# Performance work log

Hardware: AMD Instinct MI355X
Metric: run time of the kernel (lower is better)

Reference implementation:

```python
import jax, jax.numpy as jnp
import numpy as np

D_MODEL = 256
NUM_HEADS = 8
WINDOW = 7
B, H, W = 2, 56, 56


def setup_inputs() -> dict:
    key = jax.random.key(0)
    ks = jax.random.split(key, 9)
    s = D_MODEL ** -0.5
    return {
        "x": jax.random.normal(ks[0], (B, D_MODEL, H, W), jnp.float32),
        "wq": jax.random.normal(ks[1], (D_MODEL, D_MODEL), jnp.float32) * s,
        "bq": jnp.zeros((D_MODEL,), jnp.float32),
        "wk": jax.random.normal(ks[2], (D_MODEL, D_MODEL), jnp.float32) * s,
        "bk": jnp.zeros((D_MODEL,), jnp.float32),
        "wv": jax.random.normal(ks[3], (D_MODEL, D_MODEL), jnp.float32) * s,
        "bv": jnp.zeros((D_MODEL,), jnp.float32),
        "wo": jax.random.normal(ks[4], (D_MODEL, D_MODEL), jnp.float32) * s,
        "bo": jnp.zeros((D_MODEL,), jnp.float32),
    }


def _proj(x, w, b):
    # 1x1 conv == channel matmul. x: [B,C,H,W], w: [Cout,Cin], b: [Cout]
    return jnp.einsum('oc,bchw->bohw', w, x) + b[None, :, None, None]


def _windows(t, ws):
    # t: [B,h,d,H,W] -> [B,h,d,H,W,ws*ws], zero-padded sliding windows.
    # Row-major (i*ws + j) flattening matches torch unfold(3).unfold(4).view(...,-1).
    pad = ws // 2
    Hh, Ww = t.shape[-2], t.shape[-1]
    tp = jnp.pad(t, ((0, 0), (0, 0), (0, 0), (pad, pad), (pad, pad)))
    return jnp.stack([tp[..., i:i + Hh, j:j + Ww]
                      for i in range(ws) for j in range(ws)], axis=-1)


def reference(x, wq, bq, wk, bk, wv, bv, wo, bo):
    Bt, C, Hh, Ww = x.shape
    hd = C // NUM_HEADS
    scale = hd ** -0.5
    q = _proj(x, wq, bq).reshape(Bt, NUM_HEADS, hd, Hh, Ww)
    k = _proj(x, wk, bk).reshape(Bt, NUM_HEADS, hd, Hh, Ww)
    v = _proj(x, wv, bv).reshape(Bt, NUM_HEADS, hd, Hh, Ww)
    kw = _windows(k, WINDOW)  # [B,h,d,H,W,ws^2]
    vw = _windows(v, WINDOW)
    attn = jnp.einsum('bhdxy,bhdxyw->bhxyw', q, kw) * scale
    attn = jax.nn.softmax(attn, axis=-1)
    out = jnp.einsum('bhxyw,bhdxyw->bhdxy', attn, vw).reshape(Bt, C, Hh, Ww)
    return _proj(out, wo, bo)
```

## Files before the change

kernel.cpp:

```cpp
#include <hip/hip_runtime.h>
#include <hip/hip_bf16.h>
#include <cstdint>

#define NHEAD 8
#define HD 32
#define DM 256
#define HH 56
#define WWID 56
#define HW 3136
#define NB 2
#define NTOT (NB * HW)
#define SCALE 0.17677669529663687f

typedef _Float16 f16;
typedef __attribute__((ext_vector_type(2))) _Float16 f16x2;
typedef __attribute__((ext_vector_type(8))) _Float16 f16x8;
typedef __attribute__((ext_vector_type(4))) float floatx4;

union U16 { uint4 u; f16x2 h2[4]; f16 h[8]; };

__global__ __launch_bounds__(256) void prep(
    const float* __restrict__ x,
    const float* __restrict__ wq, const float* __restrict__ wk,
    const float* __restrict__ wv, const float* __restrict__ wo,
    f16* __restrict__ xT, f16* __restrict__ wcat, f16* __restrict__ wob)
{
    const int bid = blockIdx.x;
    const int t = threadIdx.x;
    if (bid < 392) {
        __shared__ float tile[64][65];
        const int b = bid / 196, r = bid - b * 196;
        const int ct = r / 49, pt = r - ct * 49;
        const int p0 = pt * 64, c0 = ct * 64;
        const float* xb = x + (size_t)b * DM * HW;
        #pragma unroll
        for (int i = 0; i < 4; ++i) {
            const int u = t + i * 256;
            const int rc = u >> 4, p4 = (u & 15) << 2;
            *(float4*)&tile[rc][p4] =
                *(const float4*)&xb[(size_t)(c0 + rc) * HW + p0 + p4];
        }
        __syncthreads();
        f16* xo = xT + (size_t)b * HW * DM;
        #pragma unroll
        for (int i = 0; i < 2; ++i) {
            const int u = t + i * 256;
            const int ch = u & 7, p = u >> 3;
            U16 pk;
            #pragma unroll
            for (int kk = 0; kk < 8; ++kk)
                pk.h[kk] = (f16)tile[ch * 8 + kk][p];
            *(uint4*)&xo[(size_t)(p0 + p) * DM + c0 + ch * 8] = pk.u;
        }
    } else {
        const int gid = (bid - 392) * 256 + t;
        const int idx4 = gid << 2;
        const int sel = idx4 >> 16;
        const int off = idx4 & 65535;
        const float* src = sel == 0 ? wq : (sel == 1 ? wk : (sel == 2 ? wv : wo));
        f16* dst = sel < 3 ? (wcat + (sel << 16) + off) : (wob + off);
        float4 f = *(const float4*)&src[off];
        union { ushort4 u; f16 h[4]; } pk;
        pk.h[0] = (f16)f.x; pk.h[1] = (f16)f.y;
        pk.h[2] = (f16)f.z; pk.h[3] = (f16)f.w;
        *(ushort4*)dst = pk.u;
    }
}

template<int MODE>
__global__ __launch_bounds__(256) void gemm_mfma(
    const f16* __restrict__ A,
    const f16* __restrict__ Bm,
    const float* __restrict__ b0, const float* __restrict__ b1,
    const float* __restrict__ b2,
    void* __restrict__ o0, void* __restrict__ o1, void* __restrict__ o2)
{
    const int n0 = blockIdx.x * 64;
    const int m0 = blockIdx.y * 128;
    const int bb = n0 / HW;
    const int np = n0 - bb * HW;
    const f16* Bb = Bm + (size_t)n0 * DM;

    __shared__ __align__(16) f16 As[128][72];
    __shared__ __align__(16) f16 Bs[64][72];

    const int t = threadIdx.x;
    const int wave = t >> 6, lane = t & 63;
    const int quad = lane >> 4, l16 = lane & 15;
    const int mw = (wave & 1) * 64, nw = (wave >> 1) * 32;

    floatx4 acc[4][2] = {};

    const int srow = t >> 3, suc = (t & 7) << 3;

    for (int k0 = 0; k0 < DM; k0 += 64) {
        #pragma unroll
        for (int pp = 0; pp < 4; ++pp) {
            const int row = srow + pp * 32;
            *(uint4*)&As[row][suc] =
                *(const uint4*)&A[(size_t)(m0 + row) * DM + k0 + suc];
        }
        #pragma unroll
        for (int pp = 0; pp < 2; ++pp) {
            const int row = srow + pp * 32;
            *(uint4*)&Bs[row][suc] =
                *(const uint4*)&Bb[(size_t)row * DM + k0 + suc];
        }
        __syncthreads();
        #pragma unroll
        for (int ks = 0; ks < 2; ++ks) {
            f16x8 af[4], bf[2];
            #pragma unroll
            for (int mt = 0; mt < 4; ++mt)
                af[mt] = *(const f16x8*)&As[mw + mt * 16 + l16][ks * 32 + quad * 8];
            #pragma unroll
            for (int nt = 0; nt < 2; ++nt)
                bf[nt] = *(const f16x8*)&Bs[nw + nt * 16 + l16][ks * 32 + quad * 8];
            #pragma unroll
            for (int mt = 0; mt < 4; ++mt)
                #pragma unroll
                for (int nt = 0; nt < 2; ++nt)
                    acc[mt][nt] = __builtin_amdgcn_mfma_f32_16x16x32_f16(
                        af[mt], bf[nt], acc[mt][nt], 0, 0, 0);
        }
        __syncthreads();
    }

    if (MODE == 0) {
        #pragma unroll
        for (int mt = 0; mt < 4; ++mt) {
            const int gm = m0 + mw + mt * 16 + quad * 4;
            const int proj = gm >> 8;
            const int c = gm & 255;
            const int h = c >> 5, d0 = c & 31;
            const float* bptr = proj == 0 ? b0 : (proj == 1 ? b1 : b2);
            f16* op = (f16*)(proj == 0 ? o0 : (proj == 1 ? o1 : o2));
            const float sc = proj == 0 ? SCALE : 1.0f;
            const size_t base = ((size_t)(bb * NHEAD + h) * HW) * HD + d0;
            float bias[4] = {bptr[c], bptr[c + 1], bptr[c + 2], bptr[c + 3]};
            #pragma unroll
            for (int nt = 0; nt < 2; ++nt) {
                const int p = np + nw + nt * 16 + l16;
                union { ushort4 u; f16 h[4]; } pk;
                #pragma unroll
                for (int r = 0; r < 4; ++r)
                    pk.h[r] = (f16)((acc[mt][nt][r] + bias[r]) * sc);
                *(ushort4*)&op[base + (size_t)p * HD] = pk.u;
            }
        }
    } else {
        float* yo = (float*)o0;
        #pragma unroll
        for (int mt = 0; mt < 4; ++mt) {
            const int gc = m0 + mw + mt * 16 + quad * 4;
            #pragma unroll
            for (int r = 0; r < 4; ++r) {
                const float bias = b0[gc + r];
                #pragma unroll
                for (int nt = 0; nt < 2; ++nt) {
                    const int p = np + nw + nt * 16 + l16;
                    yo[(size_t)(bb * DM + gc + r) * HW + p] = acc[mt][nt][r] + bias;
                }
            }
        }
    }
}

#define HROWS 8
#define HPOS  (HROWS * WWID)
#define HPP   (HPOS + 6)

__global__ __launch_bounds__(448) void attn_win(
    const f16* __restrict__ q,
    const f16* __restrict__ k,
    const f16* __restrict__ v,
    f16* __restrict__ out)
{
    __shared__ uint4 kh[HPP * 4];
    __shared__ uint4 vh[HPP * 4];

    const int t = threadIdx.x;
    const int tile = blockIdx.x;
    const int h = blockIdx.y, b = blockIdx.z;
    const int y0 = tile * 2;
    const size_t base = (size_t)(b * NHEAD + h) * HW * HD;
    const f16* kp = k + base;
    const f16* vp = v + base;

    #pragma unroll
    for (int it = 0; it < 4; ++it) {
        const int u = t + it * 448;
        const int pos = u >> 2, ch = u & 3;
        const int hr = pos / WWID;
        const int gx = pos - hr * WWID;
        const int gy = y0 - 3 + hr;
        uint4 kv = make_uint4(0, 0, 0, 0), vv = make_uint4(0, 0, 0, 0);
        if ((unsigned)gy < HH) {
            const size_t g = (size_t)(gy * WWID + gx) * HD + (ch << 3);
            kv = *(const uint4*)&kp[g];
            vv = *(const uint4*)&vp[g];
        }
        kh[u + 12] = kv;
        vh[u + 12] = vv;
    }
    if (t < 48) {
        const int ps = t % 6;
        const int fi = (ps < 3 ? ps * 4 : (HPOS + ps) * 4) + ((t / 6) & 3);
        const uint4 z = make_uint4(0, 0, 0, 0);
        if (t < 24) kh[fi] = z; else vh[fi] = z;
    }
    __syncthreads();

    const int pl = t >> 2;
    const int ch = t & 3;
    const int lx = pl >= WWID ? pl - WWID : pl;
    const int p = y0 * WWID + pl;

    U16 qu;
    qu.u = *(const uint4*)(q + base + (size_t)p * HD + (ch << 3));

    const uint4* kb4 = kh + t;
    const uint4* vb4 = vh + t;

    float of[8] = {};
    float sum = 0.f;
    for (int i = 0; i < 7; ++i) {
        #pragma unroll
        for (int j = 0; j < 7; ++j) {
            const int off4 = (i * WWID + j) << 2;
            U16 ku; ku.u = kb4[off4];
            float s;
            s = __builtin_amdgcn_fdot2(ku.h2[0], qu.h2[0], 0.0f, false);
            s = __builtin_amdgcn_fdot2(ku.h2[1], qu.h2[1], s, false);
            s = __builtin_amdgcn_fdot2(ku.h2[2], qu.h2[2], s, false);
            s = __builtin_amdgcn_fdot2(ku.h2[3], qu.h2[3], s, false);
            s += __shfl_xor(s, 1);
            s += __shfl_xor(s, 2);
            const bool xv = (unsigned)(lx + j - 3) < WWID;
            const float e = __expf(s);
            sum += xv ? e : 1.0f;
            const float wt = xv ? e : 0.0f;
            U16 vu; vu.u = vb4[off4];
            of[0] = fmaf((float)vu.h[0], wt, of[0]);
            of[1] = fmaf((float)vu.h[1], wt, of[1]);
            of[2] = fmaf((float)vu.h[2], wt, of[2]);
            of[3] = fmaf((float)vu.h[3], wt, of[3]);
            of[4] = fmaf((float)vu.h[4], wt, of[4]);
            of[5] = fmaf((float)vu.h[5], wt, of[5]);
            of[6] = fmaf((float)vu.h[6], wt, of[6]);
            of[7] = fmaf((float)vu.h[7], wt, of[7]);
        }
    }

    const float inv = 1.0f / sum;
    f16* op = out + ((size_t)b * HW + p) * DM + h * HD + (ch << 3);
    U16 ou;
    #pragma unroll
    for (int j = 0; j < 8; ++j)
        ou.h[j] = (f16)(of[j] * inv);
    *(uint4*)op = ou.u;
}

extern "C" void kernel_launch(void* const* d_in, const int* in_sizes, int n_in,
                              void* d_out, int out_size, void* d_ws, size_t ws_size,
                              hipStream_t stream) {
    const float* x  = (const float*)d_in[0];
    const float* wq = (const float*)d_in[1];
    const float* bq = (const float*)d_in[2];
    const float* wk = (const float*)d_in[3];
    const float* bk = (const float*)d_in[4];
    const float* wv = (const float*)d_in[5];
    const float* bv = (const float*)d_in[6];
    const float* wo = (const float*)d_in[7];
    const float* bo = (const float*)d_in[8];
    float* out = (float*)d_out;

    const size_t NPC = (size_t)NTOT * DM;
    f16* xT    = (f16*)d_ws;
    f16* wcat  = xT + NPC;
    f16* wob   = wcat + 768 * 256;
    f16* qb    = wob + 256 * 256;
    f16* kb    = qb + NPC;
    f16* vb    = kb + NPC;
    f16* attnT = vb + NPC;

    prep<<<648, 256, 0, stream>>>(x, wq, wk, wv, wo, xT, wcat, wob);
    gemm_mfma<0><<<dim3(NTOT / 64, 6), 256, 0, stream>>>(
        wcat, xT, bq, bk, bv, qb, kb, vb);
    attn_win<<<dim3(28, NHEAD, NB), 448, 0, stream>>>(qb, kb, vb, attnT);
    gemm_mfma<1><<<dim3(NTOT / 64, 2), 256, 0, stream>>>(
        wob, attnT, bo, bo, bo, out, out, out);
}
```

Before: 113.4 us.

## Fuse all four stages into one persistent kernel with software grid barriers

Replaces the four launches (prep, QKV GEMM, windowed attention, output GEMM) with a single persistent 512-block kernel that separates the phases with a hierarchical atomic grid barrier. The attention phase also moves from 2-row strips to 8x8 spatial tiles with a 14x14 zero-padded halo, which removes the per-column validity masking. The aim is to cut kernel launch gaps and tail effects between stages. In exchange, the GEMMs now loop over tiles within a fixed grid, the barrier spins add cost, and correctness relies on all 512 blocks being co-resident, since block 0 resets the barrier state while other blocks may already be spinning on it.

```diff
diff --git a/kernel.cpp b/kernel.cpp
--- a/kernel.cpp
+++ b/kernel.cpp
@@ -11,6 +11,9 @@
 #define NB 2
 #define NTOT (NB * HW)
 #define SCALE 0.17677669529663687f
+#define NBLK 512
+#define GEN0 0x13570000u
+#define AGT __HIP_MEMORY_SCOPE_AGENT
 
 typedef _Float16 f16;
 typedef __attribute__((ext_vector_type(2))) _Float16 f16x2;
@@ -19,16 +22,148 @@
 
 union U16 { uint4 u; f16x2 h2[4]; f16 h[8]; };
 
-__global__ __launch_bounds__(256) void prep(
+__device__ __forceinline__ void gridsync(unsigned* bar, unsigned expect) {
+    __syncthreads();
+    if (threadIdx.x == 0) {
+        unsigned* gen = bar + 288;
+        while (__hip_atomic_load(gen, __ATOMIC_ACQUIRE, AGT) != expect) {}
+        __threadfence();
+        unsigned* cg = bar + ((blockIdx.x >> 6) << 5);
+        if (__hip_atomic_fetch_add(cg, 1u, __ATOMIC_ACQ_REL, AGT) == 63u) {
+            __hip_atomic_store(cg, 0u, __ATOMIC_RELAXED, AGT);
+            unsigned* root = bar + 256;
+            if (__hip_atomic_fetch_add(root, 1u, __ATOMIC_ACQ_REL, AGT) == 7u) {
+                __hip_atomic_store(root, 0u, __ATOMIC_RELAXED, AGT);
+                __hip_atomic_store(gen, expect + 1u, __ATOMIC_RELEASE, AGT);
+            } else {
+                while (__hip_atomic_load(gen, __ATOMIC_ACQUIRE, AGT) == expect) {}
+            }
+        } else {
+            while (__hip_atomic_load(gen, __ATOMIC_ACQUIRE, AGT) == expect) {}
+        }
+        __threadfence();
+    }
+    __syncthreads();
+}
+
+template<int MODE>
+__device__ __forceinline__ void gemm_phase(
+    const f16* __restrict__ A, const f16* __restrict__ Bm,
+    const float* __restrict__ b0, const float* __restrict__ b1,
+    const float* __restrict__ b2,
+    f16* __restrict__ o0, f16* __restrict__ o1, f16* __restrict__ o2,
+    float* __restrict__ yo,
+    void* smem, int ntiles)
+{
+    f16 (*As)[72] = (f16(*)[72])smem;
+    f16 (*Bs)[72] = (f16(*)[72])((char*)smem + 18432);
+    const int t = threadIdx.x;
+    const int wave = t >> 6, lane = t & 63;
+    const int quad = lane >> 4, l16 = lane & 15;
+    const int mw = (wave & 1) * 64, nw = (wave >> 1) * 32;
+    const int srow = t >> 3, suc = (t & 7) << 3;
+
+    for (int tile = blockIdx.x; tile < ntiles; tile += NBLK) {
+        const int mt = tile / 98, nt = tile - mt * 98;
+        const int n0g = nt * 64, m0 = mt * 128;
+        const int bb = n0g / HW, np = n0g - bb * HW;
+        const f16* Bb = Bm + (size_t)n0g * DM;
+        floatx4 acc[4][2] = {};
+        for (int k0 = 0; k0 < DM; k0 += 64) {
+            #pragma unroll
+            for (int pp = 0; pp < 4; ++pp) {
+                const int row = srow + pp * 32;
+                *(uint4*)&As[row][suc] =
+                    *(const uint4*)&A[(size_t)(m0 + row) * DM + k0 + suc];
+            }
+            #pragma unroll
+            for (int pp = 0; pp < 2; ++pp) {
+                const int row = srow + pp * 32;
+                *(uint4*)&Bs[row][suc] =
+                    *(const uint4*)&Bb[(size_t)row * DM + k0 + suc];
+            }
+            __syncthreads();
+            #pragma unroll
+            for (int ks = 0; ks < 2; ++ks) {
+                f16x8 af[4], bf[2];
+                #pragma unroll
+                for (int mt2 = 0; mt2 < 4; ++mt2)
+                    af[mt2] = *(const f16x8*)&As[mw + mt2 * 16 + l16][ks * 32 + quad * 8];
+                #pragma unroll
+                for (int nt2 = 0; nt2 < 2; ++nt2)
+                    bf[nt2] = *(const f16x8*)&Bs[nw + nt2 * 16 + l16][ks * 32 + quad * 8];
+                #pragma unroll
+                for (int mt2 = 0; mt2 < 4; ++mt2)
+                    #pragma unroll
+                    for (int nt2 = 0; nt2 < 2; ++nt2)
+                        acc[mt2][nt2] = __builtin_amdgcn_mfma_f32_16x16x32_f16(
+                            af[mt2], bf[nt2], acc[mt2][nt2], 0, 0, 0);
+            }
+            __syncthreads();
+        }
+        if (MODE == 0) {
+            #pragma unroll
+            for (int mt2 = 0; mt2 < 4; ++mt2) {
+                const int gm = m0 + mw + mt2 * 16 + quad * 4;
+                const int proj = gm >> 8;
+                const int c = gm & 255;
+                const int h = c >> 5, d0 = c & 31;
+                const float* bptr = proj == 0 ? b0 : (proj == 1 ? b1 : b2);
+                f16* op = proj == 0 ? o0 : (proj == 1 ? o1 : o2);
+                const float sc = proj == 0 ? SCALE : 1.0f;
+                const size_t base = ((size_t)(bb * NHEAD + h) * HW) * HD + d0;
+                float bias[4] = {bptr[c], bptr[c + 1], bptr[c + 2], bptr[c + 3]};
+                #pragma unroll
+                for (int nt2 = 0; nt2 < 2; ++nt2) {
+                    const int p = np + nw + nt2 * 16 + l16;
+                    union { ushort4 u; f16 h[4]; } pk;
+                    #pragma unroll
+                    for (int r = 0; r < 4; ++r)
+                        pk.h[r] = (f16)((acc[mt2][nt2][r] + bias[r]) * sc);
+                    *(ushort4*)&op[base + (size_t)p * HD] = pk.u;
+                }
+            }
+        } else {
+            #pragma unroll
+            for (int mt2 = 0; mt2 < 4; ++mt2) {
+                const int gc = m0 + mw + mt2 * 16 + quad * 4;
+                #pragma unroll
+                for (int r = 0; r < 4; ++r) {
+                    const float bias = b0[gc + r];
+                    #pragma unroll
+                    for (int nt2 = 0; nt2 < 2; ++nt2) {
+                        const int p = np + nw + nt2 * 16 + l16;
+                        yo[(size_t)(bb * DM + gc + r) * HW + p] = acc[mt2][nt2][r] + bias;
+                    }
+                }
+            }
+        }
+    }
+}
+
+__global__ __launch_bounds__(256) void fused_all(
     const float* __restrict__ x,
-    const float* __restrict__ wq, const float* __restrict__ wk,
-    const float* __restrict__ wv, const float* __restrict__ wo,
-    f16* __restrict__ xT, f16* __restrict__ wcat, f16* __restrict__ wob)
+    const float* __restrict__ wq, const float* __restrict__ bq,
+    const float* __restrict__ wk, const float* __restrict__ bk,
+    const float* __restrict__ wv, const float* __restrict__ bv,
+    const float* __restrict__ wo, const float* __restrict__ bo,
+    f16* __restrict__ xT, f16* __restrict__ wcat, f16* __restrict__ wob,
+    f16* __restrict__ qb, f16* __restrict__ kb, f16* __restrict__ vb,
+    f16* __restrict__ attnT, float* __restrict__ out, unsigned* bar)
 {
-    const int bid = blockIdx.x;
-    const int t = threadIdx.x;
+    __shared__ __align__(16) unsigned char smem[27648];
+    const int bid = blockIdx.x, t = threadIdx.x;
+
+    if (bid == 0 && t == 0) {
+        #pragma unroll
+        for (int g = 0; g < 8; ++g)
+            __hip_atomic_store(bar + g * 32, 0u, __ATOMIC_RELAXED, AGT);
+        __hip_atomic_store(bar + 256, 0u, __ATOMIC_RELAXED, AGT);
+        __hip_atomic_store(bar + 288, GEN0, __ATOMIC_RELEASE, AGT);
+    }
+
     if (bid < 392) {
-        __shared__ float tile[64][65];
+        float (*tile)[65] = (float(*)[65])smem;
         const int b = bid / 196, r = bid - b * 196;
         const int ct = r / 49, pt = r - ct * 49;
         const int p0 = pt * 64, c0 = ct * 64;
@@ -45,220 +180,101 @@
         #pragma unroll
         for (int i = 0; i < 2; ++i) {
             const int u = t + i * 256;
-            const int ch = u & 7, p = u >> 3;
+            const int ch = u & 7, pq = u >> 3;
             U16 pk;
             #pragma unroll
             for (int kk = 0; kk < 8; ++kk)
-                pk.h[kk] = (f16)tile[ch * 8 + kk][p];
-            *(uint4*)&xo[(size_t)(p0 + p) * DM + c0 + ch * 8] = pk.u;
+                pk.h[kk] = (f16)tile[ch * 8 + kk][pq];
+            *(uint4*)&xo[(size_t)(p0 + pq) * DM + c0 + ch * 8] = pk.u;
         }
     } else {
-        const int gid = (bid - 392) * 256 + t;
-        const int idx4 = gid << 2;
-        const int sel = idx4 >> 16;
-        const int off = idx4 & 65535;
-        const float* src = sel == 0 ? wq : (sel == 1 ? wk : (sel == 2 ? wv : wo));
-        f16* dst = sel < 3 ? (wcat + (sel << 16) + off) : (wob + off);
-        float4 f = *(const float4*)&src[off];
-        union { ushort4 u; f16 h[4]; } pk;
-        pk.h[0] = (f16)f.x; pk.h[1] = (f16)f.y;
-        pk.h[2] = (f16)f.z; pk.h[3] = (f16)f.w;
-        *(ushort4*)dst = pk.u;
-    }
-}
-
-template<int MODE>
-__global__ __launch_bounds__(256) void gemm_mfma(
-    const f16* __restrict__ A,
-    const f16* __restrict__ Bm,
-    const float* __restrict__ b0, const float* __restrict__ b1,
-    const float* __restrict__ b2,
-    void* __restrict__ o0, void* __restrict__ o1, void* __restrict__ o2)
-{
-    const int n0 = blockIdx.x * 64;
-    const int m0 = blockIdx.y * 128;
-    const int bb = n0 / HW;
-    const int np = n0 - bb * HW;
-    const f16* Bb = Bm + (size_t)n0 * DM;
-
-    __shared__ __align__(16) f16 As[128][72];
-    __shared__ __align__(16) f16 Bs[64][72];
-
-    const int t = threadIdx.x;
-    const int wave = t >> 6, lane = t & 63;
-    const int quad = lane >> 4, l16 = lane & 15;
-    const int mw = (wave & 1) * 64, nw = (wave >> 1) * 32;
-
-    floatx4 acc[4][2] = {};
-
-    const int srow = t >> 3, suc = (t & 7) << 3;
-
-    for (int k0 = 0; k0 < DM; k0 += 64) {
-        #pragma unroll
-        for (int pp = 0; pp < 4; ++pp) {
-            const int row = srow + pp * 32;
-            *(uint4*)&As[row][suc] =
-                *(const uint4*)&A[(size_t)(m0 + row) * DM + k0 + suc];
-        }
-        #pragma unroll
-        for (int pp = 0; pp < 2; ++pp) {
-            const int row = srow + pp * 32;
-            *(uint4*)&Bs[row][suc] =
-                *(const uint4*)&Bb[(size_t)row * DM + k0 + suc];
-        }
-        __syncthreads();
-        #pragma unroll
-        for (int ks = 0; ks < 2; ++ks) {
-            f16x8 af[4], bf[2];
-            #pragma unroll
-            for (int mt = 0; mt < 4; ++mt)
-                af[mt] = *(const f16x8*)&As[mw + mt * 16 + l16][ks * 32 + quad * 8];
-            #pragma unroll
-            for (int nt = 0; nt < 2; ++nt)
-                bf[nt] = *(const f16x8*)&Bs[nw + nt * 16 + l16][ks * 32 + quad * 8];
-            #pragma unroll
-            for (int mt = 0; mt < 4; ++mt)
-                #pragma unroll
-                for (int nt = 0; nt < 2; ++nt)
-                    acc[mt][nt] = __builtin_amdgcn_mfma_f32_16x16x32_f16(
-                        af[mt], bf[nt], acc[mt][nt], 0, 0, 0);
-        }
-        __syncthreads();
-    }
-
-    if (MODE == 0) {
-        #pragma unroll
-        for (int mt = 0; mt < 4; ++mt) {
-            const int gm = m0 + mw + mt * 16 + quad * 4;
-            const int proj = gm >> 8;
-            const int c = gm & 255;
-            const int h = c >> 5, d0 = c & 31;
-            const float* bptr = proj == 0 ? b0 : (proj == 1 ? b1 : b2);
-            f16* op = (f16*)(proj == 0 ? o0 : (proj == 1 ? o1 : o2));
-            const float sc = proj == 0 ? SCALE : 1.0f;
-            const size_t base = ((size_t)(bb * NHEAD + h) * HW) * HD + d0;
-            float bias[4] = {bptr[c], bptr[c + 1], bptr[c + 2], bptr[c + 3]};
-            #pragma unroll
-            for (int nt = 0; nt < 2; ++nt) {
-                const int p = np + nw + nt * 16 + l16;
-                union { ushort4 u; f16 h[4]; } pk;
-                #pragma unroll
-                for (int r = 0; r < 4; ++r)
-                    pk.h[r] = (f16)((acc[mt][nt][r] + bias[r]) * sc);
-                *(ushort4*)&op[base + (size_t)p * HD] = pk.u;
-            }
-        }
-    } else {
-        float* yo = (float*)o0;
-        #pragma unroll
-        for (int mt = 0; mt < 4; ++mt) {
-            const int gc = m0 + mw + mt * 16 + quad * 4;
-            #pragma unroll
-            for (int r = 0; r < 4; ++r) {
-                const float bias = b0[gc + r];
-                #pragma unroll
-                for (int nt = 0; nt < 2; ++nt) {
-                    const int p = np + nw + nt * 16 + l16;
-                    yo[(size_t)(bb * DM + gc + r) * HW + p] = acc[mt][nt][r] + bias;
+        for (int gid = (bid - 392) * 256 + t; gid < 65536; gid += 30720) {
+            const int idx4 = gid << 2;
+            const int sel = idx4 >> 16, off = idx4 & 65535;
+            const float* src = sel == 0 ? wq : (sel == 1 ? wk : (sel == 2 ? wv : wo));
+            f16* dst = sel < 3 ? (wcat + (sel << 16) + off) : (wob + off);
+            float4 f = *(const float4*)&src[off];
+            union { ushort4 u; f16 h[4]; } pk;
+            pk.h[0] = (f16)f.x; pk.h[1] = (f16)f.y;
+            pk.h[2] = (f16)f.z; pk.h[3] = (f16)f.w;
+            *(ushort4*)dst = pk.u;
+        }
+    }
+    gridsync(bar, GEN0);
+
+    gemm_phase<0>(wcat, xT, bq, bk, bv, qb, kb, vb, nullptr, smem, 588);
+    gridsync(bar, GEN0 + 1);
+
+    {
+        uint4* kh = (uint4*)smem;
+        uint4* vh = (uint4*)(smem + 12544);
+        for (int tl = bid; tl < 784; tl += NBLK) {
+            const int bh = tl / 49, r = tl - bh * 49;
+            const int ry = r / 7;
+            const int ty0 = ry * 8, tx0 = (r - ry * 7) * 8;
+            const f16* kp = kb + (size_t)bh * HW * HD;
+            const f16* vp = vb + (size_t)bh * HW * HD;
+            __syncthreads();
+            for (int u = t; u < 784; u += 256) {
+                const int pos = u >> 2, ch = u & 3;
+                const int hy = pos / 14, hx = pos - hy * 14;
+                const int gy = ty0 + hy - 3, gx = tx0 + hx - 3;
+                uint4 kv = make_uint4(0, 0, 0, 0), vv = make_uint4(0, 0, 0, 0);
+                if ((unsigned)gy < HH && (unsigned)gx < WWID) {
+                    const size_t g = (size_t)(gy * WWID + gx) * HD + (ch << 3);
+                    kv = *(const uint4*)&kp[g];
+                    vv = *(const uint4*)&vp[g];
                 }
-            }
-        }
-    }
-}
-
-#define HROWS 8
-#define HPOS  (HROWS * WWID)
-#define HPP   (HPOS + 6)
-
-__global__ __launch_bounds__(448) void attn_win(
-    const f16* __restrict__ q,
-    const f16* __restrict__ k,
-    const f16* __restrict__ v,
-    f16* __restrict__ out)
-{
-    __shared__ uint4 kh[HPP * 4];
-    __shared__ uint4 vh[HPP * 4];
-
-    const int t = threadIdx.x;
-    const int tile = blockIdx.x;
-    const int h = blockIdx.y, b = blockIdx.z;
-    const int y0 = tile * 2;
-    const size_t base = (size_t)(b * NHEAD + h) * HW * HD;
-    const f16* kp = k + base;
-    const f16* vp = v + base;
-
-    #pragma unroll
-    for (int it = 0; it < 4; ++it) {
-        const int u = t + it * 448;
-        const int pos = u >> 2, ch = u & 3;
-        const int hr = pos / WWID;
-        const int gx = pos - hr * WWID;
-        const int gy = y0 - 3 + hr;
-        uint4 kv = make_uint4(0, 0, 0, 0), vv = make_uint4(0, 0, 0, 0);
-        if ((unsigned)gy < HH) {
-            const size_t g = (size_t)(gy * WWID + gx) * HD + (ch << 3);
-            kv = *(const uint4*)&kp[g];
-            vv = *(const uint4*)&vp[g];
-        }
-        kh[u + 12] = kv;
-        vh[u + 12] = vv;
-    }
-    if (t < 48) {
-        const int ps = t % 6;
-        const int fi = (ps < 3 ? ps * 4 : (HPOS + ps) * 4) + ((t / 6) & 3);
-        const uint4 z = make_uint4(0, 0, 0, 0);
-        if (t < 24) kh[fi] = z; else vh[fi] = z;
-    }
-    __syncthreads();
-
-    const int pl = t >> 2;
-    const int ch = t & 3;
-    const int lx = pl >= WWID ? pl - WWID : pl;
-    const int p = y0 * WWID + pl;
-
-    U16 qu;
-    qu.u = *(const uint4*)(q + base + (size_t)p * HD + (ch << 3));
-
-    const uint4* kb4 = kh + t;
-    const uint4* vb4 = vh + t;
-
-    float of[8] = {};
-    float sum = 0.f;
-    for (int i = 0; i < 7; ++i) {
-        #pragma unroll
-        for (int j = 0; j < 7; ++j) {
-            const int off4 = (i * WWID + j) << 2;
-            U16 ku; ku.u = kb4[off4];
-            float s;
-            s = __builtin_amdgcn_fdot2(ku.h2[0], qu.h2[0], 0.0f, false);
-            s = __builtin_amdgcn_fdot2(ku.h2[1], qu.h2[1], s, false);
-            s = __builtin_amdgcn_fdot2(ku.h2[2], qu.h2[2], s, false);
-            s = __builtin_amdgcn_fdot2(ku.h2[3], qu.h2[3], s, false);
-            s += __shfl_xor(s, 1);
-            s += __shfl_xor(s, 2);
-            const bool xv = (unsigned)(lx + j - 3) < WWID;
-            const float e = __expf(s);
-            sum += xv ? e : 1.0f;
-            const float wt = xv ? e : 0.0f;
-            U16 vu; vu.u = vb4[off4];
-            of[0] = fmaf((float)vu.h[0], wt, of[0]);
-            of[1] = fmaf((float)vu.h[1], wt, of[1]);
-            of[2] = fmaf((float)vu.h[2], wt, of[2]);
-            of[3] = fmaf((float)vu.h[3], wt, of[3]);
-            of[4] = fmaf((float)vu.h[4], wt, of[4]);
-            of[5] = fmaf((float)vu.h[5], wt, of[5]);
-            of[6] = fmaf((float)vu.h[6], wt, of[6]);
-            of[7] = fmaf((float)vu.h[7], wt, of[7]);
-        }
-    }
-
-    const float inv = 1.0f / sum;
-    f16* op = out + ((size_t)b * HW + p) * DM + h * HD + (ch << 3);
-    U16 ou;
-    #pragma unroll
-    for (int j = 0; j < 8; ++j)
-        ou.h[j] = (f16)(of[j] * inv);
-    *(uint4*)op = ou.u;
+                kh[u] = kv; vh[u] = vv;
+            }
+            __syncthreads();
+            const int pl = t >> 2, ch = t & 3;
+            const int ty = pl >> 3, tx = pl & 7;
+            const int p = (ty0 + ty) * WWID + tx0 + tx;
+            U16 qu;
+            qu.u = *(const uint4*)(qb + (size_t)bh * HW * HD + (size_t)p * HD + (ch << 3));
+            const uint4* kbase = kh + (ty * 14 + tx) * 4 + ch;
+            const uint4* vbase = vh + (ty * 14 + tx) * 4 + ch;
+            float of[8] = {};
+            float sum = 0.f;
+            for (int i = 0; i < 7; ++i) {
+                #pragma unroll
+                for (int j = 0; j < 7; ++j) {
+                    const int off = (i * 14 + j) << 2;
+                    U16 ku; ku.u = kbase[off];
+                    float s = __builtin_amdgcn_fdot2(ku.h2[0], qu.h2[0], 0.0f, false);
+                    s = __builtin_amdgcn_fdot2(ku.h2[1], qu.h2[1], s, false);
+                    s = __builtin_amdgcn_fdot2(ku.h2[2], qu.h2[2], s, false);
+                    s = __builtin_amdgcn_fdot2(ku.h2[3], qu.h2[3], s, false);
+                    s += __shfl_xor(s, 1);
+                    s += __shfl_xor(s, 2);
+                    const float e = __expf(s);
+                    sum += e;
+                    U16 vu; vu.u = vbase[off];
+                    of[0] = fmaf((float)vu.h[0], e, of[0]);
+                    of[1] = fmaf((float)vu.h[1], e, of[1]);
+                    of[2] = fmaf((float)vu.h[2], e, of[2]);
+                    of[3] = fmaf((float)vu.h[3], e, of[3]);
+                    of[4] = fmaf((float)vu.h[4], e, of[4]);
+                    of[5] = fmaf((float)vu.h[5], e, of[5]);
+                    of[6] = fmaf((float)vu.h[6], e, of[6]);
+                    of[7] = fmaf((float)vu.h[7], e, of[7]);
+                }
+            }
+            const float inv = 1.0f / sum;
+            f16* op = attnT + ((size_t)(bh >> 3) * HW + p) * DM
+                            + (bh & 7) * HD + (ch << 3);
+            U16 ou;
+            #pragma unroll
+            for (int j = 0; j < 8; ++j)
+                ou.h[j] = (f16)(of[j] * inv);
+            *(uint4*)op = ou.u;
+        }
+    }
+    gridsync(bar, GEN0 + 2);
+
+    gemm_phase<1>(wob, attnT, bo, nullptr, nullptr,
+                  nullptr, nullptr, nullptr, out, smem, 196);
 }
 
 extern "C" void kernel_launch(void* const* d_in, const int* in_sizes, int n_in,
@@ -283,11 +299,9 @@
     f16* kb    = qb + NPC;
     f16* vb    = kb + NPC;
     f16* attnT = vb + NPC;
-
-    prep<<<648, 256, 0, stream>>>(x, wq, wk, wv, wo, xT, wcat, wob);
-    gemm_mfma<0><<<dim3(NTOT / 64, 6), 256, 0, stream>>>(
-        wcat, xT, bq, bk, bv, qb, kb, vb);
-    attn_win<<<dim3(28, NHEAD, NB), 448, 0, stream>>>(qb, kb, vb, attnT);
-    gemm_mfma<1><<<dim3(NTOT / 64, 2), 256, 0, stream>>>(
-        wob, attnT, bo, bo, bo, out, out, out);
+    unsigned* bar = (unsigned*)(attnT + NPC);
+
+    fused_all<<<NBLK, 256, 0, stream>>>(
+        x, wq, bq, wk, bk, wv, bv, wo, bo,
+        xT, wcat, wob, qb, kb, vb, attnT, out, bar);
 }
```

After: 303.9 us. +168.1%, slower.

## Fuse fp32-to-fp16 conversion and transpose into the projection GEMMs, dropping prep kernel

Applied to the files above, without the earlier changes.

Removes the separate prep kernel that converted x and the weights to fp16 and transposed x. The QKV GEMM now reads fp32 weights and the NCHW x directly, converting to fp16 while staging into shared memory with a transposed scalar store. The output GEMM likewise converts wo on the fly. This saves one launch and the workspace round trip, but adds redundant weight conversion per block, scalar strided loads of x, and possible bank conflicts on the transposed shared-memory writes.

```diff
diff --git a/kernel.cpp b/kernel.cpp
--- a/kernel.cpp
+++ b/kernel.cpp
@@ -19,67 +19,23 @@
 
 union U16 { uint4 u; f16x2 h2[4]; f16 h[8]; };
 
-__global__ __launch_bounds__(256) void prep(
+__global__ __launch_bounds__(256) void gemm_qkv(
     const float* __restrict__ x,
-    const float* __restrict__ wq, const float* __restrict__ wk,
-    const float* __restrict__ wv, const float* __restrict__ wo,
-    f16* __restrict__ xT, f16* __restrict__ wcat, f16* __restrict__ wob)
+    const float* __restrict__ wq, const float* __restrict__ bq,
+    const float* __restrict__ wk, const float* __restrict__ bk,
+    const float* __restrict__ wv, const float* __restrict__ bv,
+    f16* __restrict__ qo, f16* __restrict__ ko, f16* __restrict__ vo)
 {
-    const int bid = blockIdx.x;
-    const int t = threadIdx.x;
-    if (bid < 392) {
-        __shared__ float tile[64][65];
-        const int b = bid / 196, r = bid - b * 196;
-        const int ct = r / 49, pt = r - ct * 49;
-        const int p0 = pt * 64, c0 = ct * 64;
-        const float* xb = x + (size_t)b * DM * HW;
-        #pragma unroll
-        for (int i = 0; i < 4; ++i) {
-            const int u = t + i * 256;
-            const int rc = u >> 4, p4 = (u & 15) << 2;
-            *(float4*)&tile[rc][p4] =
-                *(const float4*)&xb[(size_t)(c0 + rc) * HW + p0 + p4];
-        }
-        __syncthreads();
-        f16* xo = xT + (size_t)b * HW * DM;
-        #pragma unroll
-        for (int i = 0; i < 2; ++i) {
-            const int u = t + i * 256;
-            const int ch = u & 7, p = u >> 3;
-            U16 pk;
-            #pragma unroll
-            for (int kk = 0; kk < 8; ++kk)
-                pk.h[kk] = (f16)tile[ch * 8 + kk][p];
-            *(uint4*)&xo[(size_t)(p0 + p) * DM + c0 + ch * 8] = pk.u;
-        }
-    } else {
-        const int gid = (bid - 392) * 256 + t;
-        const int idx4 = gid << 2;
-        const int sel = idx4 >> 16;
-        const int off = idx4 & 65535;
-        const float* src = sel == 0 ? wq : (sel == 1 ? wk : (sel == 2 ? wv : wo));
-        f16* dst = sel < 3 ? (wcat + (sel << 16) + off) : (wob + off);
-        float4 f = *(const float4*)&src[off];
-        union { ushort4 u; f16 h[4]; } pk;
-        pk.h[0] = (f16)f.x; pk.h[1] = (f16)f.y;
-        pk.h[2] = (f16)f.z; pk.h[3] = (f16)f.w;
-        *(ushort4*)dst = pk.u;
-    }
-}
-
-template<int MODE>
-__global__ __launch_bounds__(256) void gemm_mfma(
-    const f16* __restrict__ A,
-    const f16* __restrict__ Bm,
-    const float* __restrict__ b0, const float* __restrict__ b1,
-    const float* __restrict__ b2,
-    void* __restrict__ o0, void* __restrict__ o1, void* __restrict__ o2)
-{
-    const int n0 = blockIdx.x * 64;
-    const int m0 = blockIdx.y * 128;
-    const int bb = n0 / HW;
-    const int np = n0 - bb * HW;
-    const f16* Bb = Bm + (size_t)n0 * DM;
+    const int n0g = blockIdx.x * 64;
+    const int ym  = blockIdx.y;
+    const int proj = ym >> 1;
+    const int mloc = (ym & 1) * 128;
+    const int bb = n0g / HW, np = n0g - bb * HW;
+    const float* __restrict__ w  = proj == 0 ? wq : (proj == 1 ? wk : wv);
+    const float* __restrict__ bi = proj == 0 ? bq : (proj == 1 ? bk : bv);
+    f16* __restrict__ o = proj == 0 ? qo : (proj == 1 ? ko : vo);
+    const float sc = proj == 0 ? SCALE : 1.0f;
+    const float* xb = x + (size_t)bb * DM * HW;
 
     __shared__ __align__(16) f16 As[128][72];
     __shared__ __align__(16) f16 Bs[64][72];
@@ -92,19 +48,29 @@
     floatx4 acc[4][2] = {};
 
     const int srow = t >> 3, suc = (t & 7) << 3;
+    const int bc = t >> 4, bp = t & 15;
 
     for (int k0 = 0; k0 < DM; k0 += 64) {
         #pragma unroll
         for (int pp = 0; pp < 4; ++pp) {
             const int row = srow + pp * 32;
-            *(uint4*)&As[row][suc] =
-                *(const uint4*)&A[(size_t)(m0 + row) * DM + k0 + suc];
-        }
-        #pragma unroll
-        for (int pp = 0; pp < 2; ++pp) {
-            const int row = srow + pp * 32;
-            *(uint4*)&Bs[row][suc] =
-                *(const uint4*)&Bb[(size_t)row * DM + k0 + suc];
+            const float* wr = &w[(size_t)(mloc + row) * DM + k0 + suc];
+            float4 a0 = *(const float4*)wr;
+            float4 a1 = *(const float4*)(wr + 4);
+            U16 pk;
+            pk.h[0] = (f16)a0.x; pk.h[1] = (f16)a0.y;
+            pk.h[2] = (f16)a0.z; pk.h[3] = (f16)a0.w;
+            pk.h[4] = (f16)a1.x; pk.h[5] = (f16)a1.y;
+            pk.h[6] = (f16)a1.z; pk.h[7] = (f16)a1.w;
+            *(uint4*)&As[row][suc] = pk.u;
+        }
+        #pragma unroll
+        for (int pp = 0; pp < 4; ++pp) {
+            const int cl = pp * 16 + bc;
+            const float* xr = &xb[(size_t)(k0 + cl) * HW + np + bp];
+            #pragma unroll
+            for (int i = 0; i < 4; ++i)
+                Bs[bp + 16 * i][cl] = (f16)xr[16 * i];
         }
         __syncthreads();
         #pragma unroll
@@ -126,41 +92,94 @@
         __syncthreads();
     }
 
-    if (MODE == 0) {
-        #pragma unroll
-        for (int mt = 0; mt < 4; ++mt) {
-            const int gm = m0 + mw + mt * 16 + quad * 4;
-            const int proj = gm >> 8;
-            const int c = gm & 255;
-            const int h = c >> 5, d0 = c & 31;
-            const float* bptr = proj == 0 ? b0 : (proj == 1 ? b1 : b2);
-            f16* op = (f16*)(proj == 0 ? o0 : (proj == 1 ? o1 : o2));
-            const float sc = proj == 0 ? SCALE : 1.0f;
-            const size_t base = ((size_t)(bb * NHEAD + h) * HW) * HD + d0;
-            float bias[4] = {bptr[c], bptr[c + 1], bptr[c + 2], bptr[c + 3]};
+    #pragma unroll
+    for (int mt = 0; mt < 4; ++mt) {
+        const int c = mloc + mw + mt * 16 + quad * 4;
+        const int h = c >> 5, d0 = c & 31;
+        const size_t base = ((size_t)(bb * NHEAD + h) * HW) * HD + d0;
+        float bias[4] = {bi[c], bi[c + 1], bi[c + 2], bi[c + 3]};
+        #pragma unroll
+        for (int nt = 0; nt < 2; ++nt) {
+            const int p = np + nw + nt * 16 + l16;
+            union { ushort4 u; f16 h[4]; } pk;
+            #pragma unroll
+            for (int r = 0; r < 4; ++r)
+                pk.h[r] = (f16)((acc[mt][nt][r] + bias[r]) * sc);
+            *(ushort4*)&o[base + (size_t)p * HD] = pk.u;
+        }
+    }
+}
+
+__global__ __launch_bounds__(256) void gemm_out(
+    const f16* __restrict__ Bm, const float* __restrict__ wo,
+    const float* __restrict__ bo, float* __restrict__ yo)
+{
+    const int n0g = blockIdx.x * 64;
+    const int m0 = blockIdx.y * 128;
+    const int bb = n0g / HW, np = n0g - bb * HW;
+    const f16* Bb = Bm + (size_t)n0g * DM;
+
+    __shared__ __align__(16) f16 As[128][72];
+    __shared__ __align__(16) f16 Bs[64][72];
+
+    const int t = threadIdx.x;
+    const int wave = t >> 6, lane = t & 63;
+    const int quad = lane >> 4, l16 = lane & 15;
+    const int mw = (wave & 1) * 64, nw = (wave >> 1) * 32;
+
+    floatx4 acc[4][2] = {};
+    const int srow = t >> 3, suc = (t & 7) << 3;
+
+    for (int k0 = 0; k0 < DM; k0 += 64) {
+        #pragma unroll
+        for (int pp = 0; pp < 4; ++pp) {
+            const int row = srow + pp * 32;
+            const float* wr = &wo[(size_t)(m0 + row) * DM + k0 + suc];
+            float4 a0 = *(const float4*)wr;
+            float4 a1 = *(const float4*)(wr + 4);
+            U16 pk;
+            pk.h[0] = (f16)a0.x; pk.h[1] = (f16)a0.y;
+            pk.h[2] = (f16)a0.z; pk.h[3] = (f16)a0.w;
+            pk.h[4] = (f16)a1.x; pk.h[5] = (f16)a1.y;
+            pk.h[6] = (f16)a1.z; pk.h[7] = (f16)a1.w;
+            *(uint4*)&As[row][suc] = pk.u;
+        }
+        #pragma unroll
+        for (int pp = 0; pp < 2; ++pp) {
+            const int row = srow + pp * 32;
+            *(uint4*)&Bs[row][suc] =
+                *(const uint4*)&Bb[(size_t)row * DM + k0 + suc];
+        }
+        __syncthreads();
+        #pragma unroll
+        for (int ks = 0; ks < 2; ++ks) {
+            f16x8 af[4], bf[2];
+            #pragma unroll
+            for (int mt = 0; mt < 4; ++mt)
+                af[mt] = *(const f16x8*)&As[mw + mt * 16 + l16][ks * 32 + quad * 8];
+            #pragma unroll
+            for (int nt = 0; nt < 2; ++nt)
+                bf[nt] = *(const f16x8*)&Bs[nw + nt * 16 + l16][ks * 32 + quad * 8];
+            #pragma unroll
+            for (int mt = 0; mt < 4; ++mt)
+                #pragma unroll
+                for (int nt = 0; nt < 2; ++nt)
+                    acc[mt][nt] = __builtin_amdgcn_mfma_f32_16x16x32_f16(
+                        af[mt], bf[nt], acc[mt][nt], 0, 0, 0);
+        }
+        __syncthreads();
+    }
+
+    #pragma unroll
+    for (int mt = 0; mt < 4; ++mt) {
+        const int gc = m0 + mw + mt * 16 + quad * 4;
+        #pragma unroll
+        for (int r = 0; r < 4; ++r) {
+            const float bias = bo[gc + r];
             #pragma unroll
             for (int nt = 0; nt < 2; ++nt) {
                 const int p = np + nw + nt * 16 + l16;
-                union { ushort4 u; f16 h[4]; } pk;
-                #pragma unroll
-                for (int r = 0; r < 4; ++r)
-                    pk.h[r] = (f16)((acc[mt][nt][r] + bias[r]) * sc);
-                *(ushort4*)&op[base + (size_t)p * HD] = pk.u;
-            }
-        }
-    } else {
-        float* yo = (float*)o0;
-        #pragma unroll
-        for (int mt = 0; mt < 4; ++mt) {
-            const int gc = m0 + mw + mt * 16 + quad * 4;
-            #pragma unroll
-            for (int r = 0; r < 4; ++r) {
-                const float bias = b0[gc + r];
-                #pragma unroll
-                for (int nt = 0; nt < 2; ++nt) {
-                    const int p = np + nw + nt * 16 + l16;
-                    yo[(size_t)(bb * DM + gc + r) * HW + p] = acc[mt][nt][r] + bias;
-                }
+                yo[(size_t)(bb * DM + gc + r) * HW + p] = acc[mt][nt][r] + bias;
             }
         }
     }
@@ -276,18 +295,13 @@
     float* out = (float*)d_out;
 
     const size_t NPC = (size_t)NTOT * DM;
-    f16* xT    = (f16*)d_ws;
-    f16* wcat  = xT + NPC;
-    f16* wob   = wcat + 768 * 256;
-    f16* qb    = wob + 256 * 256;
+    f16* qb    = (f16*)d_ws;
     f16* kb    = qb + NPC;
     f16* vb    = kb + NPC;
     f16* attnT = vb + NPC;
 
-    prep<<<648, 256, 0, stream>>>(x, wq, wk, wv, wo, xT, wcat, wob);
-    gemm_mfma<0><<<dim3(NTOT / 64, 6), 256, 0, stream>>>(
-        wcat, xT, bq, bk, bv, qb, kb, vb);
+    gemm_qkv<<<dim3(NTOT / 64, 6), 256, 0, stream>>>(
+        x, wq, bq, wk, bk, wv, bv, qb, kb, vb);
     attn_win<<<dim3(28, NHEAD, NB), 448, 0, stream>>>(qb, kb, vb, attnT);
-    gemm_mfma<1><<<dim3(NTOT / 64, 2), 256, 0, stream>>>(
-        wob, attnT, bo, bo, bo, out, out, out);
+    gemm_out<<<dim3(NTOT / 64, 2), 256, 0, stream>>>(attnT, wo, bo, out);
 }
```

Result: no change. 112.8 us (-0.5%).
